# Performance work log

Hardware: AMD Instinct MI355X
Metric: run time of the kernel (lower is better)

The kernel has to match this reference:

```python
import jax, jax.numpy as jnp
import numpy as np

B, S, HID = 4, 2048, 2048
NH, NKV, HD = 16, 4, 128  # head_dim = HID // NH
Q_SIZE, KV_SIZE = NH * HD, NKV * HD


def setup_inputs() -> dict:
    key = jax.random.key(0)
    ks = jax.random.split(key, 8)
    pos = jnp.arange(S, dtype=jnp.float32)[:, None]
    inv_freq = 1.0 / (10000.0 ** (jnp.arange(0, HD, 2, dtype=jnp.float32) / HD))  # [HD/2]
    ang = pos * inv_freq[None, :]  # [S, HD/2]
    return {
        "hidden_states": jax.random.normal(ks[0], (B, S, HID), jnp.float32),
        "rotary_pos_emb_cos": jnp.cos(ang),
        "rotary_pos_emb_sin": jnp.sin(ang),
        "w_qkv": jax.random.normal(ks[1], (HID, Q_SIZE + 2 * KV_SIZE), jnp.float32) * (HID ** -0.5),
        "b_qkv": jax.random.normal(ks[2], (Q_SIZE + 2 * KV_SIZE,), jnp.float32) * 0.02,
        "w_o": jax.random.normal(ks[3], (HID, HID), jnp.float32) * (HID ** -0.5),
        "b_o": jax.random.normal(ks[4], (HID,), jnp.float32) * 0.02,
    }


def _apply_rope(x, cos, sin):
    # x: [B, S, H, D]; cos/sin: [S, D/2]; rotate-half (non-interleaved) convention
    d2 = x.shape[-1] // 2
    x1, x2 = x[..., :d2], x[..., d2:]
    c = cos[None, :, None, :]
    s = sin[None, :, None, :]
    return jnp.concatenate([x1 * c - x2 * s, x2 * c + x1 * s], axis=-1)


def reference(hidden_states, rotary_pos_emb_cos, rotary_pos_emb_sin, w_qkv, b_qkv, w_o, b_o):
    b, s, _ = hidden_states.shape
    qkv = hidden_states @ w_qkv + b_qkv  # [B, S, Q_SIZE + 2*KV_SIZE]
    q, k, v = jnp.split(qkv, [Q_SIZE, Q_SIZE + KV_SIZE], axis=-1)
    q = q.reshape(b, s, NH, HD)
    k = k.reshape(b, s, NKV, HD)
    v = v.reshape(b, s, NKV, HD)
    q = _apply_rope(q, rotary_pos_emb_cos, rotary_pos_emb_sin)
    k = _apply_rope(k, rotary_pos_emb_cos, rotary_pos_emb_sin)
    # grouped-query attention: repeat kv heads to match query heads
    g = NH // NKV
    k = jnp.repeat(k, g, axis=2)  # [B, S, NH, HD]
    v = jnp.repeat(v, g, axis=2)
    scale = HD ** -0.5
    scores = jnp.einsum("bshd,bthd->bhst", q, k) * scale  # [B, NH, S, S]
    probs = jax.nn.softmax(scores, axis=-1)
    out = jnp.einsum("bhst,bthd->bshd", probs, v)  # [B, S, NH, HD]
    out = out.reshape(b, s, NH * HD)
    return out @ w_o + b_o
```

## Files before the change

### kernel.cpp

```cpp
#include <hip/hip_runtime.h>
#include <math.h>

#define B_N   4
#define S_N   2048
#define HID_N 2048
#define NH_N  16
#define NKV_N 4
#define HD_N  128
#define QSZ   2048
#define KVSZ  512
#define QKVN  3072
#define M_N   8192

typedef __bf16 bf16;
typedef __bf16 bf16x8 __attribute__((ext_vector_type(8)));
typedef float  f32x4  __attribute__((ext_vector_type(4)));

#define GLL16(gp, lp)                                                          \
  __builtin_amdgcn_global_load_lds(                                            \
      (const __attribute__((address_space(1))) void*)(gp),                     \
      (__attribute__((address_space(3))) void*)(lp), 16, 0, 0)

__device__ __forceinline__ f32x4 mfma16(bf16x8 a, bf16x8 b, f32x4 c) {
  return __builtin_amdgcn_mfma_f32_16x16x32_bf16(a, b, c, 0, 0, 0);
}

__global__ __launch_bounds__(256) void conv_bf16_kernel(
    const float* __restrict__ X, bf16* __restrict__ Y)
{
  size_t i = ((size_t)blockIdx.x * 256 + threadIdx.x) * 8;
  float4 a = *(const float4*)&X[i];
  float4 b = *(const float4*)&X[i + 4];
  union { bf16 h[8]; uint4 u; } pk;
  pk.h[0] = (bf16)a.x; pk.h[1] = (bf16)a.y; pk.h[2] = (bf16)a.z; pk.h[3] = (bf16)a.w;
  pk.h[4] = (bf16)b.x; pk.h[5] = (bf16)b.y; pk.h[6] = (bf16)b.z; pk.h[7] = (bf16)b.w;
  *(uint4*)&Y[i] = pk.u;
}

__global__ __launch_bounds__(256) void convT_kernel(
    const float* __restrict__ W, bf16* __restrict__ Wt, int K, int N)
{
  __shared__ __attribute__((aligned(16))) bf16 tile[64 * 68];
  const int n0 = blockIdx.x * 64, k0 = blockIdx.y * 64;
#pragma unroll
  for (int it = 0; it < 4; ++it) {
    int idx = it * 256 + threadIdx.x;
    int r = idx >> 4, c4 = (idx & 15) << 2;
    float4 v = *(const float4*)&W[(size_t)(k0 + r) * N + n0 + c4];
    union { bf16 h[4]; unsigned long long u; } pk;
    pk.h[0] = (bf16)v.x; pk.h[1] = (bf16)v.y; pk.h[2] = (bf16)v.z; pk.h[3] = (bf16)v.w;
    *(unsigned long long*)&tile[r * 68 + c4] = pk.u;
  }
  __syncthreads();
#pragma unroll
  for (int it = 0; it < 4; ++it) {
    int idx = it * 256 + threadIdx.x;
    int rn = idx >> 4, ck4 = (idx & 15) << 2;
    union { bf16 h[4]; unsigned long long u; } pk;
#pragma unroll
    for (int i = 0; i < 4; ++i) pk.h[i] = tile[(ck4 + i) * 68 + rn];
    *(unsigned long long*)&Wt[(size_t)(n0 + rn) * K + k0 + ck4] = pk.u;
  }
}

template <bool OUT_BF16>
__global__ __launch_bounds__(256, 2) void gemm_bf16_kernel(
    const bf16* __restrict__ A, const bf16* __restrict__ Bt,
    const float* __restrict__ bias, void* __restrict__ Cout,
    int M, int N, int K)
{
  __shared__ __attribute__((aligned(16))) bf16 As[128 * 32];
  __shared__ __attribute__((aligned(16))) bf16 Bs[128 * 32];

  const int tid  = threadIdx.x;
  const int lane = tid & 63, wv = tid >> 6;
  const int quad = lane >> 4, ln = lane & 15;
  const int row0 = blockIdx.y * 128, col0 = blockIdx.x * 128;
  const int wr = (wv >> 1) * 64, wc = (wv & 1) * 64;

  f32x4 acc[4][4];
  const f32x4 zero = {0.f, 0.f, 0.f, 0.f};
#pragma unroll
  for (int mt = 0; mt < 4; ++mt)
#pragma unroll
    for (int nt = 0; nt < 4; ++nt) acc[mt][nt] = zero;

  const int s0 = wv * 128 + lane;
  const bf16* gA0 = A  + (size_t)(row0 + (s0 >> 2)) * K + (s0 & 3) * 8;
  const bf16* gA1 = gA0 + 16 * (size_t)K;
  const bf16* gB0 = Bt + (size_t)(col0 + (s0 >> 2)) * K + (s0 & 3) * 8;
  const bf16* gB1 = gB0 + 16 * (size_t)K;
  bf16* lA0 = As + (size_t)wv * 1024;
  bf16* lA1 = lA0 + 512;
  bf16* lB0 = Bs + (size_t)wv * 1024;
  bf16* lB1 = lB0 + 512;

  for (int k0 = 0; k0 < K; k0 += 32) {
    GLL16(gA0 + k0, lA0);
    GLL16(gA1 + k0, lA1);
    GLL16(gB0 + k0, lB0);
    GLL16(gB1 + k0, lB1);
    __syncthreads();

    bf16x8 a[4], b[4];
#pragma unroll
    for (int mt = 0; mt < 4; ++mt)
      a[mt] = *(const bf16x8*)&As[(wr + mt * 16 + ln) * 32 + quad * 8];
#pragma unroll
    for (int nt = 0; nt < 4; ++nt)
      b[nt] = *(const bf16x8*)&Bs[(wc + nt * 16 + ln) * 32 + quad * 8];
#pragma unroll
    for (int mt = 0; mt < 4; ++mt)
#pragma unroll
      for (int nt = 0; nt < 4; ++nt)
        acc[mt][nt] = mfma16(a[mt], b[nt], acc[mt][nt]);
    __syncthreads();
  }

#pragma unroll
  for (int nt = 0; nt < 4; ++nt) {
    const int c = col0 + wc + nt * 16 + ln;
    const float bv = bias[c];
#pragma unroll
    for (int mt = 0; mt < 4; ++mt) {
#pragma unroll
      for (int r = 0; r < 4; ++r) {
        const int rr = row0 + wr + mt * 16 + quad * 4 + r;
        const float v = acc[mt][nt][r] + bv;
        if (OUT_BF16) ((bf16*)Cout)[(size_t)rr * N + c] = (bf16)v;
        else          ((float*)Cout)[(size_t)rr * N + c] = v;
      }
    }
  }
}

__global__ __launch_bounds__(256) void rope_repack_kernel(
    const bf16* __restrict__ qkvB, const float* __restrict__ cosb,
    const float* __restrict__ sinb, bf16* __restrict__ Qb, bf16* __restrict__ Kb)
{
  int idx = blockIdx.x * 256 + threadIdx.x;
  int j  = idx & 63;
  int m  = (idx >> 6) & (M_N - 1);
  int hh = idx >> 19;
  int b = m >> 11, s = m & (S_N - 1);
  float c  = cosb[s * 64 + j];
  float sn = sinb[s * 64 + j];
  if (hh < NH_N) {
    const bf16* src = qkvB + (size_t)m * QKVN + hh * HD_N;
    float x1 = (float)src[j], x2 = (float)src[j + 64];
    bf16* dst = Qb + ((size_t)(b * NH_N + hh) * S_N + s) * HD_N;
    const float qs = 0.08838834764831845f * 1.4426950408889634f;
    dst[j]      = (bf16)((x1 * c - x2 * sn) * qs);
    dst[j + 64] = (bf16)((x2 * c + x1 * sn) * qs);
  } else {
    int kh = hh - NH_N;
    const bf16* src = qkvB + (size_t)m * QKVN + QSZ + kh * HD_N;
    float x1 = (float)src[j], x2 = (float)src[j + 64];
    bf16* dst = Kb + ((size_t)(b * NKV_N + kh) * S_N + s) * HD_N;
    dst[j]      = (bf16)(x1 * c - x2 * sn);
    dst[j + 64] = (bf16)(x2 * c + x1 * sn);
  }
}

__global__ __launch_bounds__(256) void transposeV_kernel(
    const bf16* __restrict__ qkvB, bf16* __restrict__ Vt)
{
  __shared__ __attribute__((aligned(16))) bf16 tile[64 * 136];
  const int s0 = blockIdx.x * 64;
  const int bkh = blockIdx.y;
  const int b = bkh >> 2, kh = bkh & 3;
#pragma unroll
  for (int it = 0; it < 4; ++it) {
    int ci = it * 256 + threadIdx.x;
    int r = ci >> 4, c = ci & 15;
    uint4 v = *(const uint4*)&qkvB[(size_t)(b * S_N + s0 + r) * QKVN +
                                   QSZ + KVSZ + kh * HD_N + c * 8];
    *(uint4*)&tile[r * 136 + c * 8] = v;
  }
  __syncthreads();
#pragma unroll
  for (int it = 0; it < 4; ++it) {
    int ci = it * 256 + threadIdx.x;
    int d = ci >> 3, c = ci & 7;
    union { bf16 h[8]; uint4 u; } pk;
#pragma unroll
    for (int i = 0; i < 8; ++i) pk.h[i] = tile[(c * 8 + i) * 136 + d];
    *(uint4*)&Vt[((size_t)bkh * HD_N + d) * S_N + s0 + c * 8] = pk.u;
  }
}

__global__ __launch_bounds__(256, 3) void attn_mfma_kernel(
    const bf16* __restrict__ Qb, const bf16* __restrict__ Kb,
    const bf16* __restrict__ Vt, bf16* __restrict__ Ob)
{
  __shared__ __attribute__((aligned(16))) bf16 Ks[2][32 * 128];
  __shared__ __attribute__((aligned(16))) bf16 Vs[2][128 * 32];
  __shared__ __attribute__((aligned(16))) bf16 Ps[128 * 40];

  const int tid  = threadIdx.x;
  const int lane = tid & 63, wv = tid >> 6;
  const int quad = lane >> 4, ln = lane & 15;

  const int gid = blockIdx.x;
  const int xcd = gid & 7, sl = gid >> 3;
  const int grp = xcd * 2 + (sl >> 6);
  const int within = sl & 63;
  const int b = grp >> 2, kh = grp & 3;
  const int h = kh * 4 + (within >> 4);
  const int q0 = (within & 15) * 128;

  const bf16* Qg = Qb + ((size_t)(b * NH_N + h) * S_N + q0) * HD_N;
  const bf16* Kg = Kb + (size_t)(b * NKV_N + kh) * S_N * HD_N;
  const bf16* Vg = Vt + (size_t)(b * NKV_N + kh) * HD_N * S_N;

  bf16x8 aq[2][4];
#pragma unroll
  for (int g = 0; g < 2; ++g) {
    const bf16* qrow = Qg + (size_t)((wv * 2 + g) * 16 + ln) * HD_N;
#pragma unroll
    for (int dc = 0; dc < 4; ++dc)
      aq[g][dc] = *(const bf16x8*)&qrow[(dc * 4 + quad) * 8];
  }

  const bf16* kga[2];
  const bf16* vga[2];
#pragma unroll
  for (int t = 0; t < 2; ++t) {
    int slot = (t * 4 + wv) * 64 + lane;
    int row = slot >> 4, cc = slot & 15;
    int csrc = (cc & 8) | ((cc & 7) ^ (row & 7));
    kga[t] = Kg + (size_t)row * 128 + csrc * 8;
    int dv = slot >> 2, ccv = slot & 3;
    int csv = ccv ^ (dv & 3);
    vga[t] = Vg + (size_t)dv * S_N + csv * 8;
  }

#pragma unroll
  for (int t = 0; t < 2; ++t) GLL16(kga[t], &Ks[0][(t * 4 + wv) * 512]);
#pragma unroll
  for (int t = 0; t < 2; ++t) GLL16(vga[t], &Vs[0][(t * 4 + wv) * 512]);

  bf16x8 bones;
#pragma unroll
  for (int j = 0; j < 8; ++j) bones[j] = (ln == 0) ? (bf16)1.0f : (bf16)0.0f;

  f32x4 accO[2][8];
  const f32x4 zero = {0.f, 0.f, 0.f, 0.f};
#pragma unroll
  for (int g = 0; g < 2; ++g)
#pragma unroll
    for (int dt = 0; dt < 8; ++dt) accO[g][dt] = zero;
  f32x4 accL[2] = {zero, zero};

  __syncthreads();

  int cur = 0;
  for (int kt = 0; kt < S_N; kt += 32, cur ^= 1) {
    const int nkt = kt + 32;
    if (nkt < S_N) {
#pragma unroll
      for (int t = 0; t < 2; ++t)
        GLL16(kga[t] + (size_t)nkt * 128, &Ks[cur ^ 1][(t * 4 + wv) * 512]);
#pragma unroll
      for (int t = 0; t < 2; ++t)
        GLL16(vga[t] + nkt, &Vs[cur ^ 1][(t * 4 + wv) * 512]);
    }
    const bf16* Kc = Ks[cur];
    const bf16* Vc = Vs[cur];

    f32x4 accS[2][2];
#pragma unroll
    for (int g = 0; g < 2; ++g)
#pragma unroll
      for (int nt = 0; nt < 2; ++nt) accS[g][nt] = zero;
#pragma unroll
    for (int nt = 0; nt < 2; ++nt) {
      const int kp = nt * 16 + ln;
#pragma unroll
      for (int dc = 0; dc < 4; ++dc) {
        int c = dc * 4 + quad;
        int cs = (c & 8) | ((c & 7) ^ (kp & 7));
        bf16x8 bk = *(const bf16x8*)&Kc[kp * 128 + cs * 8];
        accS[0][nt] = mfma16(aq[0][dc], bk, accS[0][nt]);
        accS[1][nt] = mfma16(aq[1][dc], bk, accS[1][nt]);
      }
    }

#pragma unroll
    for (int g = 0; g < 2; ++g)
#pragma unroll
      for (int r = 0; r < 4; ++r) {
        const int q = (wv * 2 + g) * 16 + quad * 4 + r;
        bf16* pr = &Ps[q * 40 + ln];
        pr[0]  = (bf16)__builtin_amdgcn_exp2f(accS[g][0][r]);
        pr[16] = (bf16)__builtin_amdgcn_exp2f(accS[g][1][r]);
      }

    bf16x8 ap[2];
#pragma unroll
    for (int g = 0; g < 2; ++g) {
      ap[g] = *(const bf16x8*)&Ps[((wv * 2 + g) * 16 + ln) * 40 + quad * 8];
      accL[g] = mfma16(ap[g], bones, accL[g]);
    }
#pragma unroll
    for (int dt = 0; dt < 8; ++dt) {
      const int d = dt * 16 + ln;
      int cs = quad ^ (d & 3);
      bf16x8 bv = *(const bf16x8*)&Vc[d * 32 + cs * 8];
      accO[0][dt] = mfma16(ap[0], bv, accO[0][dt]);
      accO[1][dt] = mfma16(ap[1], bv, accO[1][dt]);
    }

    __syncthreads();
  }

#pragma unroll
  for (int g = 0; g < 2; ++g)
#pragma unroll
    for (int r = 0; r < 4; ++r) {
      const float l = __shfl(accL[g][r], lane & 48);
      const float inv = 1.f / l;
      const int q = q0 + (wv * 2 + g) * 16 + quad * 4 + r;
      const size_t base = ((size_t)b * S_N + q) * HID_N + h * HD_N;
#pragma unroll
      for (int dt = 0; dt < 8; ++dt)
        Ob[base + dt * 16 + ln] = (bf16)(accO[g][dt][r] * inv);
    }
}

extern "C" void kernel_launch(void* const* d_in, const int* in_sizes, int n_in,
                              void* d_out, int out_size, void* d_ws, size_t ws_size,
                              hipStream_t stream) {
  const float* hidden = (const float*)d_in[0];
  const float* cosb   = (const float*)d_in[1];
  const float* sinb   = (const float*)d_in[2];
  const float* w_qkv  = (const float*)d_in[3];
  const float* b_qkv  = (const float*)d_in[4];
  const float* w_o    = (const float*)d_in[5];
  const float* b_o    = (const float*)d_in[6];
  float* out = (float*)d_out;

  char* w = (char*)d_ws;
  bf16* qkvB  = (bf16*)(w);
  bf16* Qb    = (bf16*)(w + 50331648);
  bf16* Kb    = (bf16*)(w + 83886080);
  bf16* Vt    = (bf16*)(w + 92274688);
  bf16* wqkvT = (bf16*)(w + 100663296);
  bf16* woT   = (bf16*)(w + 113246208);
  bf16* hidB  = (bf16*)(w + 121634816);
  bf16* attnB = hidB;

  conv_bf16_kernel<<<(M_N * HID_N) / (256 * 8), 256, 0, stream>>>(hidden, hidB);
  convT_kernel<<<dim3(QKVN / 64, HID_N / 64), 256, 0, stream>>>(w_qkv, wqkvT, HID_N, QKVN);
  convT_kernel<<<dim3(HID_N / 64, HID_N / 64), 256, 0, stream>>>(w_o, woT, HID_N, HID_N);

  gemm_bf16_kernel<true><<<dim3(QKVN / 128, M_N / 128), 256, 0, stream>>>(
      hidB, wqkvT, b_qkv, qkvB, M_N, QKVN, HID_N);

  rope_repack_kernel<<<(M_N * (NH_N + NKV_N) * 64) / 256, 256, 0, stream>>>(
      qkvB, cosb, sinb, Qb, Kb);
  transposeV_kernel<<<dim3(S_N / 64, B_N * NKV_N), 256, 0, stream>>>(qkvB, Vt);

  attn_mfma_kernel<<<1024, 256, 0, stream>>>(Qb, Kb, Vt, attnB);

  gemm_bf16_kernel<false><<<dim3(HID_N / 128, M_N / 128), 256, 0, stream>>>(
      attnB, woT, b_o, out, M_N, HID_N, HID_N);
}
```

Before: 548.4 us.

## Double-buffer GEMM LDS tiles and change V tile swizzle in attention

The GEMM kernel now double-buffers its A and B LDS tiles, issuing the global-to-LDS loads for the next K step before computing on the current one, with one barrier per iteration instead of two. This is meant to overlap global memory latency with MFMA work, at the cost of twice the LDS per block, which may reduce occupancy under launch_bounds(256,2). Separately, the attention V tile XOR swizzle now uses (d>>1)&3 instead of d&3, applied consistently on write and read, to cut LDS bank conflicts on the V reads.

```diff
diff --git a/kernel.cpp b/kernel.cpp
--- a/kernel.cpp
+++ b/kernel.cpp
@@ -69,8 +69,8 @@
     const float* __restrict__ bias, void* __restrict__ Cout,
     int M, int N, int K)
 {
-  __shared__ __attribute__((aligned(16))) bf16 As[128 * 32];
-  __shared__ __attribute__((aligned(16))) bf16 Bs[128 * 32];
+  __shared__ __attribute__((aligned(16))) bf16 As[2][128 * 32];
+  __shared__ __attribute__((aligned(16))) bf16 Bs[2][128 * 32];
 
   const int tid  = threadIdx.x;
   const int lane = tid & 63, wv = tid >> 6;
@@ -90,30 +90,37 @@
   const bf16* gA1 = gA0 + 16 * (size_t)K;
   const bf16* gB0 = Bt + (size_t)(col0 + (s0 >> 2)) * K + (s0 & 3) * 8;
   const bf16* gB1 = gB0 + 16 * (size_t)K;
-  bf16* lA0 = As + (size_t)wv * 1024;
-  bf16* lA1 = lA0 + 512;
-  bf16* lB0 = Bs + (size_t)wv * 1024;
-  bf16* lB1 = lB0 + 512;
-
-  for (int k0 = 0; k0 < K; k0 += 32) {
-    GLL16(gA0 + k0, lA0);
-    GLL16(gA1 + k0, lA1);
-    GLL16(gB0 + k0, lB0);
-    GLL16(gB1 + k0, lB1);
-    __syncthreads();
+  const int lofs0 = wv * 1024, lofs1 = lofs0 + 512;
+
+  GLL16(gA0, &As[0][lofs0]);
+  GLL16(gA1, &As[0][lofs1]);
+  GLL16(gB0, &Bs[0][lofs0]);
+  GLL16(gB1, &Bs[0][lofs1]);
+  __syncthreads();
+
+  int cur = 0;
+  for (int k0 = 0; k0 < K; k0 += 32, cur ^= 1) {
+    const int nk = k0 + 32;
+    if (nk < K) {
+      GLL16(gA0 + nk, &As[cur ^ 1][lofs0]);
+      GLL16(gA1 + nk, &As[cur ^ 1][lofs1]);
+      GLL16(gB0 + nk, &Bs[cur ^ 1][lofs0]);
+      GLL16(gB1 + nk, &Bs[cur ^ 1][lofs1]);
+    }
 
     bf16x8 a[4], b[4];
 #pragma unroll
     for (int mt = 0; mt < 4; ++mt)
-      a[mt] = *(const bf16x8*)&As[(wr + mt * 16 + ln) * 32 + quad * 8];
+      a[mt] = *(const bf16x8*)&As[cur][(wr + mt * 16 + ln) * 32 + quad * 8];
 #pragma unroll
     for (int nt = 0; nt < 4; ++nt)
-      b[nt] = *(const bf16x8*)&Bs[(wc + nt * 16 + ln) * 32 + quad * 8];
+      b[nt] = *(const bf16x8*)&Bs[cur][(wc + nt * 16 + ln) * 32 + quad * 8];
 #pragma unroll
     for (int mt = 0; mt < 4; ++mt)
 #pragma unroll
       for (int nt = 0; nt < 4; ++nt)
         acc[mt][nt] = mfma16(a[mt], b[nt], acc[mt][nt]);
+
     __syncthreads();
   }
 
@@ -231,7 +238,7 @@
     int csrc = (cc & 8) | ((cc & 7) ^ (row & 7));
     kga[t] = Kg + (size_t)row * 128 + csrc * 8;
     int dv = slot >> 2, ccv = slot & 3;
-    int csv = ccv ^ (dv & 3);
+    int csv = ccv ^ ((dv >> 1) & 3);
     vga[t] = Vg + (size_t)dv * S_N + csv * 8;
   }
 
@@ -305,7 +312,7 @@
 #pragma unroll
     for (int dt = 0; dt < 8; ++dt) {
       const int d = dt * 16 + ln;
-      int cs = quad ^ (d & 3);
+      int cs = quad ^ ((d >> 1) & 3);
       bf16x8 bv = *(const bf16x8*)&Vc[d * 32 + cs * 8];
       accO[0][dt] = mfma16(ap[0], bv, accO[0][dt]);
       accO[1][dt] = mfma16(ap[1], bv, accO[1][dt]);
```

Measured after the change: 544.6 us. About the same (-0.7%).
